# Performance work log

Measured on AMD Instinct MI355X. Metric: run time of the kernel, lower is better.

Reference implementation:

```python
import jax, jax.numpy as jnp
import numpy as np

Z, N = 14336, 4096  # down_proj: intermediate -> hidden (Llama-3-8B scale)


def setup_inputs() -> dict:
    key = jax.random.key(0)
    k1, k2 = jax.random.split(key)
    x = jax.random.normal(k1, (1, 1, Z), dtype=jnp.float32)  # decode-time GEMV input
    W_t = jax.random.normal(k2, (Z, N), dtype=jnp.float32) * 0.02  # W.T, contiguous [Z, N]
    thresh = jnp.array([0.9], dtype=jnp.float32)
    return {"x": x, "W_t": W_t, "thresh": thresh}


def reference(x, W_t, thresh):
    # W_norm = ||orig_W[:, z]||_2 = row norms of W_t, shape [Z]
    W_norm = jnp.linalg.norm(W_t, axis=1)
    # abs_mul_leq: keep input coord z iff |x_z| * W_norm_z >= thresh
    m = (jnp.abs(x) * W_norm) >= thresh  # [1, 1, Z]
    # y[n] = sum_z mask_z * x_z * W_t[z, n]  (gather-transposed GEMV)
    xm = jnp.where(m, x, jnp.zeros((), dtype=x.dtype))
    return jnp.einsum('bsz,zn->bsn', xm, W_t)  # [1, 1, N]
```

## Files before the change

### kernel.cpp

```cpp
#include <hip/hip_runtime.h>
#include <cmath>


#define ZDIM   14336
#define NDIM   4096
#define NF4    1024
#define ZCHUNK 28
#define NBLK   512

__global__ __launch_bounds__(256, 2) void fused_norm_gemv(
    const float* __restrict__ x,
    const float* __restrict__ Wt,
    const float* __restrict__ thresh,
    float* __restrict__ part) {
  const int t    = threadIdx.x;
  const int lane = t & 63;
  const int wv   = t >> 6;
  const int z0   = blockIdx.x * ZCHUNK;

  __shared__ float xs[ZCHUNK];
  __shared__ float red[2][4];

  if (t < ZCHUNK) xs[t] = x[z0 + t];
  __syncthreads();
  const float th = thresh[0];

  const float4* __restrict__ W4 = reinterpret_cast<const float4*>(Wt) + t;

  float4 acc0 = {0,0,0,0}, acc1 = {0,0,0,0}, acc2 = {0,0,0,0}, acc3 = {0,0,0,0};

  float4 s0a,s0b,s0c,s0d, s1a,s1b,s1c,s1d, s2a,s2b,s2c,s2d, s3a,s3b,s3c,s3d;

#define LOADROW(S, r) do {                                                   \
    const float4* p_ = W4 + (size_t)(z0 + (r)) * NF4;                        \
    S##a = p_[0]; S##b = p_[256]; S##c = p_[512]; S##d = p_[768];            \
  } while (0)

#define FMA16(S, xz) do {                                                    \
    acc0.x = fmaf(xz, S##a.x, acc0.x); acc0.y = fmaf(xz, S##a.y, acc0.y);    \
    acc0.z = fmaf(xz, S##a.z, acc0.z); acc0.w = fmaf(xz, S##a.w, acc0.w);    \
    acc1.x = fmaf(xz, S##b.x, acc1.x); acc1.y = fmaf(xz, S##b.y, acc1.y);    \
    acc1.z = fmaf(xz, S##b.z, acc1.z); acc1.w = fmaf(xz, S##b.w, acc1.w);    \
    acc2.x = fmaf(xz, S##c.x, acc2.x); acc2.y = fmaf(xz, S##c.y, acc2.y);    \
    acc2.z = fmaf(xz, S##c.z, acc2.z); acc2.w = fmaf(xz, S##c.w, acc2.w);    \
    acc3.x = fmaf(xz, S##d.x, acc3.x); acc3.y = fmaf(xz, S##d.y, acc3.y);    \
    acc3.z = fmaf(xz, S##d.z, acc3.z); acc3.w = fmaf(xz, S##d.w, acc3.w);    \
  } while (0)

#define ROW(CUR, PREV, r) do {                                               \
    float ss = CUR##a.x*CUR##a.x + CUR##a.y*CUR##a.y                         \
             + CUR##a.z*CUR##a.z + CUR##a.w*CUR##a.w                         \
             + CUR##b.x*CUR##b.x + CUR##b.y*CUR##b.y                         \
             + CUR##b.z*CUR##b.z + CUR##b.w*CUR##b.w                         \
             + CUR##c.x*CUR##c.x + CUR##c.y*CUR##c.y                         \
             + CUR##c.z*CUR##c.z + CUR##c.w*CUR##c.w                         \
             + CUR##d.x*CUR##d.x + CUR##d.y*CUR##d.y                         \
             + CUR##d.z*CUR##d.z + CUR##d.w*CUR##d.w;                        \
    ss += __shfl_xor(ss, 1, 64);                                             \
    ss += __shfl_xor(ss, 2, 64);                                             \
    ss += __shfl_xor(ss, 4, 64);                                             \
    ss += __shfl_xor(ss, 8, 64);                                             \
    ss += __shfl_xor(ss, 16, 64);                                            \
    ss += __shfl_xor(ss, 32, 64);                                            \
    if (lane == 0) red[(r) & 1][wv] = ss;                                    \
    if (mP) FMA16(PREV, xzP);                   \
    if ((r) + 3 < ZCHUNK) LOADROW(PREV, (r) + 3);    \
    asm volatile("s_waitcnt lgkmcnt(0)" ::: "memory");                       \
    __builtin_amdgcn_s_barrier();                                            \
    asm volatile("" ::: "memory");                                           \
    const float n2 = red[(r) & 1][0] + red[(r) & 1][1]                       \
                   + red[(r) & 1][2] + red[(r) & 1][3];                      \
    const float xz = xs[(r)];                                                \
    mP  = (fabsf(xz) * sqrtf(n2) >= th);                                     \
    xzP = xz;                                                                \
  } while (0)

  LOADROW(s0, 0);
  LOADROW(s1, 1);
  LOADROW(s2, 2);

  float xzP = 0.0f;
  bool  mP  = false;

  for (int rb = 0; rb < 24; rb += 4) {
    ROW(s0, s3, rb + 0);
    ROW(s1, s0, rb + 1);
    ROW(s2, s1, rb + 2);
    ROW(s3, s2, rb + 3);
  }
  ROW(s0, s3, 24);
  ROW(s1, s0, 25);
  ROW(s2, s1, 26);
  ROW(s3, s2, 27);
  if (mP) FMA16(s3, xzP);

  float4* p4 = (float4*)part + (size_t)blockIdx.x * NF4;
  p4[t]       = acc0;
  p4[t + 256] = acc1;
  p4[t + 512] = acc2;
  p4[t + 768] = acc3;
#undef ROW
#undef FMA16
#undef LOADROW
}

__global__ __launch_bounds__(256) void reduce_parts(
    const float* __restrict__ part, float* __restrict__ y) {
  const int t  = threadIdx.x;
  const int c  = t & 3;
  const int jg = t >> 2;
  const int c4 = blockIdx.x * 4 + c;
  const float4* __restrict__ p4 = (const float4*)part;

  float4 s = {0.f, 0.f, 0.f, 0.f};
  #pragma unroll
  for (int jj = 0; jj < 8; ++jj) {
    const float4 v = p4[(size_t)(jg * 8 + jj) * NF4 + c4];
    s.x += v.x; s.y += v.y; s.z += v.z; s.w += v.w;
  }

  __shared__ float4 sh[64][4];
  sh[jg][c] = s;
  __syncthreads();
  if (jg < 8) {
    #pragma unroll
    for (int k = 1; k < 8; ++k) {
      const float4 v = sh[jg + 8 * k][c];
      s.x += v.x; s.y += v.y; s.z += v.z; s.w += v.w;
    }
    sh[jg][c] = s;
  }
  __syncthreads();
  if (jg == 0) {
    #pragma unroll
    for (int k = 1; k < 8; ++k) {
      const float4 v = sh[k][c];
      s.x += v.x; s.y += v.y; s.z += v.z; s.w += v.w;
    }
    ((float4*)y)[c4] = s;
  }
}

extern "C" void kernel_launch(void* const* d_in, const int* in_sizes, int n_in,
                              void* d_out, int out_size, void* d_ws, size_t ws_size,
                              hipStream_t stream) {
  const float* x      = (const float*)d_in[0];
  const float* Wt     = (const float*)d_in[1];
  const float* thresh = (const float*)d_in[2];
  float* y            = (float*)d_out;
  float* part         = (float*)d_ws;

  fused_norm_gemv<<<NBLK, 256, 0, stream>>>(x, Wt, thresh, part);
  reduce_parts<<<NF4 / 4, 256, 0, stream>>>(part, y);
}
```

Measured before the change: 46.20 us.

## Stage weight rows through an LDS ring via direct global-to-LDS loads

Weight rows no longer go through register prefetch. They are now streamed into a 4-deep shared-memory ring with global_load_lds, using vmcnt waits and barriers to pace the pipeline, and each row is then read back from LDS for the norm and the FMA. The goal is to free registers and issue async loads that fill LDS directly, keeping more bytes in flight. In exchange it uses 64KB of LDS per block, which may limit occupancy, and adds an extra LDS read per row.

```diff
diff --git a/kernel.cpp b/kernel.cpp
--- a/kernel.cpp
+++ b/kernel.cpp
@@ -7,6 +7,10 @@
 #define NF4    1024
 #define ZCHUNK 28
 #define NBLK   512
+#define DEPTH  4
+
+typedef const __attribute__((address_space(1))) float* gas_fp;
+typedef __attribute__((address_space(3))) float* las_fp;
 
 __global__ __launch_bounds__(256, 2) void fused_norm_gemv(
     const float* __restrict__ x,
@@ -18,23 +22,31 @@
   const int wv   = t >> 6;
   const int z0   = blockIdx.x * ZCHUNK;
 
+  __shared__ float ring[DEPTH][NDIM];
   __shared__ float xs[ZCHUNK];
   __shared__ float red[2][4];
 
   if (t < ZCHUNK) xs[t] = x[z0 + t];
+  const float th = thresh[0];
   __syncthreads();
-  const float th = thresh[0];
 
-  const float4* __restrict__ W4 = reinterpret_cast<const float4*>(Wt) + t;
+  const int soff = wv * 1024 + lane * 4;
+
+#define STAGE(slot, zrow) do {                                               \
+    const float* gsrc = Wt + (size_t)(zrow) * NDIM + soff;                   \
+    float* ldst = &ring[slot][soff];                                         \
+    __builtin_amdgcn_global_load_lds((gas_fp)(gsrc      ), (las_fp)(ldst      ), 16, 0, 0); \
+    __builtin_amdgcn_global_load_lds((gas_fp)(gsrc + 256), (las_fp)(ldst + 256), 16, 0, 0); \
+    __builtin_amdgcn_global_load_lds((gas_fp)(gsrc + 512), (las_fp)(ldst + 512), 16, 0, 0); \
+    __builtin_amdgcn_global_load_lds((gas_fp)(gsrc + 768), (las_fp)(ldst + 768), 16, 0, 0); \
+  } while (0)
+
+  STAGE(0, z0 + 0);
+  STAGE(1, z0 + 1);
+  STAGE(2, z0 + 2);
 
   float4 acc0 = {0,0,0,0}, acc1 = {0,0,0,0}, acc2 = {0,0,0,0}, acc3 = {0,0,0,0};
-
-  float4 s0a,s0b,s0c,s0d, s1a,s1b,s1c,s1d, s2a,s2b,s2c,s2d, s3a,s3b,s3c,s3d;
-
-#define LOADROW(S, r) do {                                                   \
-    const float4* p_ = W4 + (size_t)(z0 + (r)) * NF4;                        \
-    S##a = p_[0]; S##b = p_[256]; S##c = p_[512]; S##d = p_[768];            \
-  } while (0)
+  float4 Aa, Ab, Ac, Ad, Ba, Bb, Bc, Bd;
 
 #define FMA16(S, xz) do {                                                    \
     acc0.x = fmaf(xz, S##a.x, acc0.x); acc0.y = fmaf(xz, S##a.y, acc0.y);    \
@@ -47,7 +59,20 @@
     acc3.z = fmaf(xz, S##d.z, acc3.z); acc3.w = fmaf(xz, S##d.w, acc3.w);    \
   } while (0)
 
-#define ROW(CUR, PREV, r) do {                                               \
+#define ROW(r, VM, CUR, PRV, DO_STAGE, DO_FMA) do {                          \
+    asm volatile("s_waitcnt vmcnt(" #VM ")" ::: "memory");                   \
+    __builtin_amdgcn_s_barrier();                                            \
+    asm volatile("" ::: "memory");                                           \
+    if (DO_STAGE) STAGE(((r) + 3) & (DEPTH - 1), z0 + (r) + 3);              \
+    const float4* r4 = (const float4*)&ring[(r) & (DEPTH - 1)][0];           \
+    CUR##a = r4[t]; CUR##b = r4[t + 256];                                    \
+    CUR##c = r4[t + 512]; CUR##d = r4[t + 768];                              \
+    if (DO_FMA) {                                                            \
+      const int pp = ((r) + 1) & 1;                                          \
+      const float n2 = red[pp][0] + red[pp][1] + red[pp][2] + red[pp][3];    \
+      const float xz = xs[(r) - 1];                                          \
+      if (fabsf(xz) * sqrtf(n2) >= th) FMA16(PRV, xz);                       \
+    }                                                                        \
     float ss = CUR##a.x*CUR##a.x + CUR##a.y*CUR##a.y                         \
              + CUR##a.z*CUR##a.z + CUR##a.w*CUR##a.w                         \
              + CUR##b.x*CUR##b.x + CUR##b.y*CUR##b.y                         \
@@ -63,36 +88,25 @@
     ss += __shfl_xor(ss, 16, 64);                                            \
     ss += __shfl_xor(ss, 32, 64);                                            \
     if (lane == 0) red[(r) & 1][wv] = ss;                                    \
-    if (mP) FMA16(PREV, xzP);                   \
-    if ((r) + 3 < ZCHUNK) LOADROW(PREV, (r) + 3);    \
     asm volatile("s_waitcnt lgkmcnt(0)" ::: "memory");                       \
-    __builtin_amdgcn_s_barrier();                                            \
-    asm volatile("" ::: "memory");                                           \
-    const float n2 = red[(r) & 1][0] + red[(r) & 1][1]                       \
-                   + red[(r) & 1][2] + red[(r) & 1][3];                      \
-    const float xz = xs[(r)];                                                \
-    mP  = (fabsf(xz) * sqrtf(n2) >= th);                                     \
-    xzP = xz;                                                                \
   } while (0)
 
-  LOADROW(s0, 0);
-  LOADROW(s1, 1);
-  LOADROW(s2, 2);
+  ROW(0, 8, A, B, 1, 0);
+  for (int rb = 1; rb <= 23; rb += 2) {
+    ROW(rb,     8, B, A, 1, 1);
+    ROW(rb + 1, 8, A, B, 1, 1);
+  }
+  ROW(25, 8, B, A, 0, 1);
+  ROW(26, 4, A, B, 0, 1);
+  ROW(27, 0, B, A, 0, 1);
 
-  float xzP = 0.0f;
-  bool  mP  = false;
-
-  for (int rb = 0; rb < 24; rb += 4) {
-    ROW(s0, s3, rb + 0);
-    ROW(s1, s0, rb + 1);
-    ROW(s2, s1, rb + 2);
-    ROW(s3, s2, rb + 3);
+  __builtin_amdgcn_s_barrier();
+  asm volatile("" ::: "memory");
+  {
+    const float n2 = red[1][0] + red[1][1] + red[1][2] + red[1][3];
+    const float xz = xs[27];
+    if (fabsf(xz) * sqrtf(n2) >= th) FMA16(B, xz);
   }
-  ROW(s0, s3, 24);
-  ROW(s1, s0, 25);
-  ROW(s2, s1, 26);
-  ROW(s3, s2, 27);
-  if (mP) FMA16(s3, xzP);
 
   float4* p4 = (float4*)part + (size_t)blockIdx.x * NF4;
   p4[t]       = acc0;
@@ -101,7 +115,7 @@
   p4[t + 768] = acc3;
 #undef ROW
 #undef FMA16
-#undef LOADROW
+#undef STAGE
 }
 
 __global__ __launch_bounds__(256) void reduce_parts(
```

Result: faster. 44.21 us (-4.3%).

## Assign whole rows per wave to drop per-row block barriers

Applied to the files above, without the earlier changes.

Each wave now processes complete rows of W, so the row norm is computed with intra-wave shuffles instead of an LDS reduction plus block barrier per row. Blocks grow to 512 threads covering 56 rows, and the 8 waves' accumulators are combined in LDS before writing, halving the number of partial vectors the second kernel reduces. The large per-thread register footprint (accumulators plus two row buffers) risks register pressure or spills at the requested occupancy.

```diff
diff --git a/kernel.cpp b/kernel.cpp
--- a/kernel.cpp
+++ b/kernel.cpp
@@ -2,13 +2,15 @@
 #include <cmath>
 
 
-#define ZDIM   14336
-#define NDIM   4096
-#define NF4    1024
-#define ZCHUNK 28
-#define NBLK   512
+#define ZDIM 14336
+#define NDIM 4096
+#define NF4  1024
+#define TPB  512
+#define NBLK 256
+#define RPB  (ZDIM / NBLK)
+#define RPW  (RPB / 8)
 
-__global__ __launch_bounds__(256, 2) void fused_norm_gemv(
+__global__ __launch_bounds__(TPB, 2) void fused_norm_gemv(
     const float* __restrict__ x,
     const float* __restrict__ Wt,
     const float* __restrict__ thresh,
@@ -16,92 +18,95 @@
   const int t    = threadIdx.x;
   const int lane = t & 63;
   const int wv   = t >> 6;
-  const int z0   = blockIdx.x * ZCHUNK;
+  const int zw   = blockIdx.x * RPB + wv * RPW;
 
-  __shared__ float xs[ZCHUNK];
-  __shared__ float red[2][4];
+  const float th = thresh[0];
+  const float4* __restrict__ W4 = reinterpret_cast<const float4*>(Wt) + lane;
 
-  if (t < ZCHUNK) xs[t] = x[z0 + t];
-  __syncthreads();
-  const float th = thresh[0];
+  float4 acc[16];
+  #pragma unroll
+  for (int j = 0; j < 16; ++j) acc[j] = make_float4(0.f, 0.f, 0.f, 0.f);
 
-  const float4* __restrict__ W4 = reinterpret_cast<const float4*>(Wt) + t;
-
-  float4 acc0 = {0,0,0,0}, acc1 = {0,0,0,0}, acc2 = {0,0,0,0}, acc3 = {0,0,0,0};
-
-  float4 s0a,s0b,s0c,s0d, s1a,s1b,s1c,s1d, s2a,s2b,s2c,s2d, s3a,s3b,s3c,s3d;
+  float4 A[16], B[16];
 
 #define LOADROW(S, r) do {                                                   \
-    const float4* p_ = W4 + (size_t)(z0 + (r)) * NF4;                        \
-    S##a = p_[0]; S##b = p_[256]; S##c = p_[512]; S##d = p_[768];            \
+    const float4* p_ = W4 + (size_t)(zw + (r)) * NF4;                        \
+    _Pragma("unroll")                                                        \
+    for (int j = 0; j < 16; ++j) S[j] = p_[j * 64];                          \
   } while (0)
 
-#define FMA16(S, xz) do {                                                    \
-    acc0.x = fmaf(xz, S##a.x, acc0.x); acc0.y = fmaf(xz, S##a.y, acc0.y);    \
-    acc0.z = fmaf(xz, S##a.z, acc0.z); acc0.w = fmaf(xz, S##a.w, acc0.w);    \
-    acc1.x = fmaf(xz, S##b.x, acc1.x); acc1.y = fmaf(xz, S##b.y, acc1.y);    \
-    acc1.z = fmaf(xz, S##b.z, acc1.z); acc1.w = fmaf(xz, S##b.w, acc1.w);    \
-    acc2.x = fmaf(xz, S##c.x, acc2.x); acc2.y = fmaf(xz, S##c.y, acc2.y);    \
-    acc2.z = fmaf(xz, S##c.z, acc2.z); acc2.w = fmaf(xz, S##c.w, acc2.w);    \
-    acc3.x = fmaf(xz, S##d.x, acc3.x); acc3.y = fmaf(xz, S##d.y, acc3.y);    \
-    acc3.z = fmaf(xz, S##d.z, acc3.z); acc3.w = fmaf(xz, S##d.w, acc3.w);    \
-  } while (0)
-
-#define ROW(CUR, PREV, r) do {                                               \
-    float ss = CUR##a.x*CUR##a.x + CUR##a.y*CUR##a.y                         \
-             + CUR##a.z*CUR##a.z + CUR##a.w*CUR##a.w                         \
-             + CUR##b.x*CUR##b.x + CUR##b.y*CUR##b.y                         \
-             + CUR##b.z*CUR##b.z + CUR##b.w*CUR##b.w                         \
-             + CUR##c.x*CUR##c.x + CUR##c.y*CUR##c.y                         \
-             + CUR##c.z*CUR##c.z + CUR##c.w*CUR##c.w                         \
-             + CUR##d.x*CUR##d.x + CUR##d.y*CUR##d.y                         \
-             + CUR##d.z*CUR##d.z + CUR##d.w*CUR##d.w;                        \
+#define COMPUTE(S, r) do {                                                   \
+    float ss = 0.f;                                                          \
+    _Pragma("unroll")                                                        \
+    for (int j = 0; j < 16; ++j)                                             \
+      ss += S[j].x * S[j].x + S[j].y * S[j].y                                \
+          + S[j].z * S[j].z + S[j].w * S[j].w;                               \
     ss += __shfl_xor(ss, 1, 64);                                             \
     ss += __shfl_xor(ss, 2, 64);                                             \
     ss += __shfl_xor(ss, 4, 64);                                             \
     ss += __shfl_xor(ss, 8, 64);                                             \
     ss += __shfl_xor(ss, 16, 64);                                            \
-    ss += __shfl_xor(ss, 32, 64);                                            \
-    if (lane == 0) red[(r) & 1][wv] = ss;                                    \
-    if (mP) FMA16(PREV, xzP);                   \
-    if ((r) + 3 < ZCHUNK) LOADROW(PREV, (r) + 3);    \
-    asm volatile("s_waitcnt lgkmcnt(0)" ::: "memory");                       \
-    __builtin_amdgcn_s_barrier();                                            \
-    asm volatile("" ::: "memory");                                           \
-    const float n2 = red[(r) & 1][0] + red[(r) & 1][1]                       \
-                   + red[(r) & 1][2] + red[(r) & 1][3];                      \
-    const float xz = xs[(r)];                                                \
-    mP  = (fabsf(xz) * sqrtf(n2) >= th);                                     \
-    xzP = xz;                                                                \
+    ss += __shfl_xor(ss, 32, 64);    \
+    const float xz = x[zw + (r)];                                            \
+    if (fabsf(xz) * sqrtf(ss) >= th) {              \
+      _Pragma("unroll")                                                      \
+      for (int j = 0; j < 16; ++j) {                                         \
+        acc[j].x = fmaf(xz, S[j].x, acc[j].x);                               \
+        acc[j].y = fmaf(xz, S[j].y, acc[j].y);                               \
+        acc[j].z = fmaf(xz, S[j].z, acc[j].z);                               \
+        acc[j].w = fmaf(xz, S[j].w, acc[j].w);                               \
+      }                                                                      \
+    }                                                                        \
   } while (0)
 
-  LOADROW(s0, 0);
-  LOADROW(s1, 1);
-  LOADROW(s2, 2);
+  LOADROW(A, 0);
+  LOADROW(B, 1);
+  COMPUTE(A, 0);
+  LOADROW(A, 2);
+  COMPUTE(B, 1);
+  LOADROW(B, 3);
+  COMPUTE(A, 2);
+  LOADROW(A, 4);
+  COMPUTE(B, 3);
+  LOADROW(B, 5);
+  COMPUTE(A, 4);
+  LOADROW(A, 6);
+  COMPUTE(B, 5);
+  COMPUTE(A, 6);
+#undef LOADROW
+#undef COMPUTE
 
-  float xzP = 0.0f;
-  bool  mP  = false;
+  __shared__ float4 lds4[4][NF4];
 
-  for (int rb = 0; rb < 24; rb += 4) {
-    ROW(s0, s3, rb + 0);
-    ROW(s1, s0, rb + 1);
-    ROW(s2, s1, rb + 2);
-    ROW(s3, s2, rb + 3);
+  if (wv < 4) {
+    #pragma unroll
+    for (int j = 0; j < 16; ++j) lds4[wv][lane + 64 * j] = acc[j];
   }
-  ROW(s0, s3, 24);
-  ROW(s1, s0, 25);
-  ROW(s2, s1, 26);
-  ROW(s3, s2, 27);
-  if (mP) FMA16(s3, xzP);
+  __syncthreads();
+  if (wv >= 4) {
+    #pragma unroll
+    for (int j = 0; j < 16; ++j) {
+      float4 v = lds4[wv - 4][lane + 64 * j];
+      v.x += acc[j].x; v.y += acc[j].y; v.z += acc[j].z; v.w += acc[j].w;
+      lds4[wv - 4][lane + 64 * j] = v;
+    }
+  }
+  __syncthreads();
 
   float4* p4 = (float4*)part + (size_t)blockIdx.x * NF4;
-  p4[t]       = acc0;
-  p4[t + 256] = acc1;
-  p4[t + 512] = acc2;
-  p4[t + 768] = acc3;
-#undef ROW
-#undef FMA16
-#undef LOADROW
+  #pragma unroll
+  for (int j = 0; j < 2; ++j) {
+    const int c4 = t + j * 512;
+    float4 s  = lds4[0][c4];
+    const float4 v1 = lds4[1][c4];
+    const float4 v2 = lds4[2][c4];
+    const float4 v3 = lds4[3][c4];
+    s.x += v1.x + v2.x + v3.x;
+    s.y += v1.y + v2.y + v3.y;
+    s.z += v1.z + v2.z + v3.z;
+    s.w += v1.w + v2.w + v3.w;
+    p4[c4] = s;
+  }
 }
 
 __global__ __launch_bounds__(256) void reduce_parts(
@@ -114,8 +119,8 @@
 
   float4 s = {0.f, 0.f, 0.f, 0.f};
   #pragma unroll
-  for (int jj = 0; jj < 8; ++jj) {
-    const float4 v = p4[(size_t)(jg * 8 + jj) * NF4 + c4];
+  for (int jj = 0; jj < 4; ++jj) {
+    const float4 v = p4[(size_t)(jg * 4 + jj) * NF4 + c4];
     s.x += v.x; s.y += v.y; s.z += v.z; s.w += v.w;
   }
 
@@ -150,6 +155,6 @@
   float* y            = (float*)d_out;
   float* part         = (float*)d_ws;
 
-  fused_norm_gemv<<<NBLK, 256, 0, stream>>>(x, Wt, thresh, part);
+  fused_norm_gemv<<<NBLK, TPB, 0, stream>>>(x, Wt, thresh, part);
   reduce_parts<<<NF4 / 4, 256, 0, stream>>>(part, y);
 }
```

Result: faster. 44.52 us (-3.6%).
